# Kernel tuning notes

Hardware: AMD Instinct MI355X
Metric: run time of the kernel (lower is better)

## Reference

```python
import jax, jax.numpy as jnp
import numpy as np

B, D_IN, H, V_TOT, T = 131072, 128, 256, 6, 6  # total_vocab = vocab_size+1 = 6


def setup_inputs() -> dict:
    key = jax.random.key(0)
    ks = jax.random.split(key, 16)
    s = 0.02
    return {
        "x": jax.random.normal(ks[0], (B, D_IN), jnp.float32),
        "W_enc": jax.random.normal(ks[1], (D_IN, H), jnp.float32) * s,
        "b_enc": jnp.zeros((H,), jnp.float32),
        "W_embed": jax.random.normal(ks[2], (V_TOT, H), jnp.float32) * s,
        "b_embed": jnp.zeros((H,), jnp.float32),
        "W_z": jax.random.normal(ks[3], (2 * H, H), jnp.float32) * s,
        "b_z": jnp.zeros((H,), jnp.float32),
        "W_r": jax.random.normal(ks[4], (2 * H, H), jnp.float32) * s,
        "b_r": jnp.zeros((H,), jnp.float32),
        "W_h": jax.random.normal(ks[5], (2 * H, H), jnp.float32) * s,
        "b_h": jnp.zeros((H,), jnp.float32),
        "W_out": jax.random.normal(ks[6], (H, V_TOT), jnp.float32) * s,
        "b_out": jnp.zeros((V_TOT,), jnp.float32),
        "start_embed": jax.random.normal(ks[7], (H,), jnp.float32) * 0.01,
    }


def reference(x, W_enc, b_enc, W_embed, b_embed, W_z, b_z, W_r, b_r, W_h, b_h,
              W_out, b_out, start_embed):
    h0 = x @ W_enc + b_enc                      # encoder: (B, H)
    bsz = h0.shape[0]
    keys = jax.random.split(jax.random.key(42), T)

    def gru(xin, h):
        c = jnp.concatenate([xin, h], axis=-1)
        z = jax.nn.sigmoid(c @ W_z + b_z)
        r = jax.nn.sigmoid(c @ W_r + b_r)
        cr = jnp.concatenate([xin, r * h], axis=-1)
        h_t = jnp.tanh(cr @ W_h + b_h)
        return (1 - z) * h + z * h_t

    def step(carry, key_t):
        h, prev_embed, total_lp, stopped, lengths = carry
        h = gru(prev_embed, h)
        logits = h @ W_out + b_out              # (B, V_TOT)
        token = jax.random.categorical(key_t, logits)  # training=True sampling
        logp = jax.nn.log_softmax(logits)
        active = (~stopped).astype(logits.dtype)
        lp = jnp.take_along_axis(logp, token[:, None], axis=1)[:, 0] * active
        total_lp = total_lp + lp
        onehot = jax.nn.one_hot(token, V_TOT, dtype=logits.dtype) * active[:, None]
        is_stop = token == (V_TOT - 1)
        lengths = lengths + ((~stopped) & (~is_stop)).astype(jnp.int32)
        stopped = stopped | is_stop
        prev_embed = jax.lax.stop_gradient(onehot) @ W_embed + b_embed
        return (h, prev_embed, total_lp, stopped, lengths), onehot

    init = (h0,
            jnp.broadcast_to(start_embed, (bsz, H)),
            jnp.zeros((bsz,), h0.dtype),
            jnp.zeros((bsz,), bool),
            jnp.zeros((bsz,), jnp.int32))
    (h, _, total_log_prob, _, lengths), onehots = jax.lax.scan(step, init, keys)
    # onehots: (T, B, V_TOT) -> message (B, T*V_TOT)
    message = jnp.transpose(onehots, (1, 0, 2)).reshape(bsz, T * V_TOT)
    return message, total_log_prob, lengths
```

## Files before the change

### kernel.cpp

```cpp
#include <hip/hip_runtime.h>
#include <stdint.h>

#define NB   131072
#define DIN  128
#define HD   256
#define VT   6
#define TS   6
#define BM   32
#define NTH  256

typedef __attribute__((ext_vector_type(8))) short bfrag;
typedef __attribute__((ext_vector_type(4))) short bh4;
typedef __attribute__((ext_vector_type(4))) float f32x4;

struct Keys { uint32_t a[6]; uint32_t b[6]; };

#define HPS(p, kc, nt, lp, j) ((((p) * 8 + (kc)) * 1040) + (nt) * 512 + (lp) * 8 + (j))

__host__ __device__ inline void tf2x32(uint32_t k0, uint32_t k1,
                                       uint32_t c0, uint32_t c1,
                                       uint32_t& o0, uint32_t& o1) {
  uint32_t ks2 = k0 ^ k1 ^ 0x1BD11BDAu;
  uint32_t x0 = c0 + k0, x1 = c1 + k1;
#define TFR(d) { x0 += x1; x1 = (x1 << (d)) | (x1 >> (32 - (d))); x1 ^= x0; }
  TFR(13) TFR(15) TFR(26) TFR(6)
  x0 += k1;  x1 += ks2 + 1u;
  TFR(17) TFR(29) TFR(16) TFR(24)
  x0 += ks2; x1 += k0 + 2u;
  TFR(13) TFR(15) TFR(26) TFR(6)
  x0 += k0;  x1 += k1 + 3u;
  TFR(17) TFR(29) TFR(16) TFR(24)
  x0 += k1;  x1 += ks2 + 4u;
  TFR(13) TFR(15) TFR(26) TFR(6)
  x0 += ks2; x1 += k0 + 5u;
#undef TFR
  o0 = x0; o1 = x1;
}

__device__ __forceinline__ unsigned short f2bf(float x) {
  uint32_t b = __float_as_uint(x);
  uint32_t r = b + 0x7FFFu + ((b >> 16) & 1u);
  return (unsigned short)(r >> 16);
}
__device__ __forceinline__ float bf2f(unsigned short u) {
  return __uint_as_float(((uint32_t)u) << 16);
}
__device__ __forceinline__ float sigf(float v) { return 1.0f / (1.0f + expf(-v)); }

#define MFMA16(a, b, c) __builtin_amdgcn_mfma_f32_16x16x32_bf16((a), (b), (c), 0, 0, 0)

__device__ __forceinline__ f32x4 prod6(const bfrag A[3], bfrag B0, bfrag B1, bfrag B2,
                                       f32x4 c) {
  c = MFMA16(A[0], B0, c);
  c = MFMA16(A[0], B1, c);
  c = MFMA16(A[1], B0, c);
  c = MFMA16(A[1], B1, c);
  c = MFMA16(A[0], B2, c);
  c = MFMA16(A[2], B0, c);
  return c;
}

__global__ void pre_kernel(const float* __restrict__ W_enc,
                           const float* __restrict__ W_embed,
                           const float* __restrict__ b_embed,
                           const float* __restrict__ start_embed,
                           const float* __restrict__ W_z, const float* __restrict__ b_z,
                           const float* __restrict__ W_r, const float* __restrict__ b_r,
                           const float* __restrict__ W_h, const float* __restrict__ b_h,
                           const float* __restrict__ W_out,
                           float* __restrict__ pre,
                           unsigned short* __restrict__ encf,
                           unsigned short* __restrict__ zf,
                           unsigned short* __restrict__ rf,
                           unsigned short* __restrict__ hf,
                           unsigned short* __restrict__ woutf) {
  const int bid = blockIdx.x;
  if (bid < 24) {
    __shared__ float xin[HD];
    const int c = bid & 7, g = bid >> 3, j = threadIdx.x;
    float v;
    if (c < 6)       v = W_embed[c * HD + j] + b_embed[j];
    else if (c == 6) v = b_embed[j];
    else             v = start_embed[j];
    xin[j] = v;
    __syncthreads();
    const float* Wg = (g == 0) ? W_z : (g == 1) ? W_r : W_h;
    const float* bg = (g == 0) ? b_z : (g == 1) ? b_r : b_h;
    float acc = bg[j];
    for (int k = 0; k < HD; ++k) acc += xin[k] * Wg[k * HD + j];
    pre[(g * 8 + c) * HD + j] = acc;
    return;
  }
  if (bid >= 136) {
    int id2 = (bid - 136) * 256 + threadIdx.x;
    int kc = id2 >> 6, lane = id2 & 63;
    int m = lane & 15, k0 = kc * 32 + ((lane >> 4) & 3) * 8;
    __align__(16) unsigned short P[3][8];
#pragma unroll
    for (int j = 0; j < 8; ++j) {
      float w = (m < VT) ? W_out[(size_t)(k0 + j) * VT + m] : 0.f;
      unsigned short h1 = f2bf(w);  float r1 = w - bf2f(h1);
      unsigned short h2 = f2bf(r1); float r2 = r1 - bf2f(h2);
      P[0][j] = h1; P[1][j] = h2; P[2][j] = f2bf(r2);
    }
    for (int p = 0; p < 3; ++p) {
      unsigned short* d = woutf + ((size_t)(p * 8 + kc) * 512) + (size_t)lane * 8;
      *(uint4*)d = *(const uint4*)P[p];
    }
    return;
  }
  int id = (bid - 24) * 256 + threadIdx.x;
  const float* src; unsigned short* dst; int kc, mt, lane, KC, krow0;
  if (id < 4096) {
    lane = id & 63; mt = (id >> 6) & 15; kc = id >> 10;
    src = W_enc; dst = encf; KC = 4; krow0 = 0;
  } else {
    int rem = id - 4096; int g = rem >> 13; int rr = rem & 8191;
    lane = rr & 63; mt = (rr >> 6) & 15; kc = rr >> 10;
    src = (g == 0) ? W_z : (g == 1) ? W_r : W_h;
    dst = (g == 0) ? zf  : (g == 1) ? rf  : hf;
    KC = 8; krow0 = 256;
  }
  const int m  = mt * 16 + (lane & 15);
  const int k0 = kc * 32 + ((lane >> 4) & 3) * 8;
  __align__(16) unsigned short P[3][8];
#pragma unroll
  for (int j = 0; j < 8; ++j) {
    float w = src[(size_t)(krow0 + k0 + j) * HD + m];
    unsigned short h1 = f2bf(w);  float r1 = w - bf2f(h1);
    unsigned short h2 = f2bf(r1); float r2 = r1 - bf2f(h2);
    P[0][j] = h1; P[1][j] = h2; P[2][j] = f2bf(r2);
  }
  for (int p = 0; p < 3; ++p) {
    unsigned short* d = dst + ((size_t)(p * KC + kc) * 16 + mt) * 512 + (size_t)lane * 8;
    *(uint4*)d = *(const uint4*)P[p];
  }
}

template<int KC, int NG>
__device__ __forceinline__ void gemm_pass(const unsigned short* __restrict__ f0,
                                          const unsigned short* __restrict__ f1,
                                          const unsigned short* hp_s,
                                          int wave, int lane,
                                          f32x4 acc0[4][2], f32x4 acc1[4][2]) {
#pragma unroll 1
  for (int kc = 0; kc < KC; ++kc) {
    bfrag B[3][2];
#pragma unroll
    for (int p = 0; p < 3; ++p)
#pragma unroll
      for (int nt = 0; nt < 2; ++nt)
        B[p][nt] = *(const bfrag*)&hp_s[HPS(p, kc, nt, lane, 0)];
#pragma unroll
    for (int mtl = 0; mtl < 4; ++mtl) {
      const int fo = (kc * 16 + wave * 4 + mtl) * 512 + lane * 8;
      bfrag A0[3], A1[3];
#pragma unroll
      for (int p = 0; p < 3; ++p) A0[p] = *(const bfrag*)(f0 + fo + p * (KC * 8192));
      if (NG == 2) {
#pragma unroll
        for (int p = 0; p < 3; ++p) A1[p] = *(const bfrag*)(f1 + fo + p * (KC * 8192));
      }
#pragma unroll
      for (int nt = 0; nt < 2; ++nt) {
        acc0[mtl][nt] = prod6(A0, B[0][nt], B[1][nt], B[2][nt], acc0[mtl][nt]);
        if (NG == 2)
          acc1[mtl][nt] = prod6(A1, B[0][nt], B[1][nt], B[2][nt], acc1[mtl][nt]);
      }
    }
  }
}

__device__ __forceinline__ void gen_gumbel(float* __restrict__ gmb, int s, int b0,
                                           int tile, int lane,
                                           uint32_t ka, uint32_t kb) {
  uint32_t basej = (uint32_t)(b0 + tile * 16) * 6u;
#pragma unroll
  for (int rep = 0; rep < 2; ++rep) {
    int d = rep * 64 + lane;
    if (d < 96) {
      uint32_t o0, o1;
      tf2x32(ka, kb, 0u, basej + (uint32_t)d, o0, o1);
      uint32_t bits = o0 ^ o1;
      float f = __uint_as_float((bits >> 9) | 0x3f800000u) - 1.0f;
      float u = (f > 0.f) ? f : 1.175494350822288e-38f;
      float lg1 = (float)log((double)u);
      float lg2 = (float)log((double)(-lg1));
      gmb[((s & 1) * 32 + tile * 16 + d / 6) * 6 + (d % 6)] = -lg2;
    }
  }
}

__launch_bounds__(NTH, 2)
__global__ void main_kernel(const float* __restrict__ x,
                            const float* __restrict__ b_enc,
                            const float* __restrict__ b_out,
                            const float* __restrict__ pre,
                            const unsigned short* __restrict__ encf,
                            const unsigned short* __restrict__ zf,
                            const unsigned short* __restrict__ rf,
                            const unsigned short* __restrict__ hf,
                            const unsigned short* __restrict__ woutf,
                            float* __restrict__ out, Keys keys) {
  __shared__ __align__(16) unsigned short hp_s[3 * 8 * 1040];
  __shared__ float gmb_s[2 * 32 * 6];
  __shared__ float boutL[16];
  __shared__ unsigned state[BM];
  __shared__ float tlp[BM];

  const int tid = threadIdx.x;
  const int wave = tid >> 6, lane = tid & 63;
  const int ln = lane & 15, qk = lane >> 4;
  const int b0 = blockIdx.x * BM;

  if (tid < 16) boutL[tid] = (tid < VT) ? b_out[tid] : 0.f;
  if (tid < BM) { state[tid] = 7u; tlp[tid] = 0.f; }

  for (int i = tid; i < BM * DIN; i += NTH) {
    int row = i >> 7, k = i & 127;
    float v = x[(size_t)(b0 + row) * DIN + k];
    unsigned short h1 = f2bf(v);  float r1 = v - bf2f(h1);
    unsigned short h2 = f2bf(r1); float r2 = r1 - bf2f(h2);
    int kc = k >> 5, nt = row >> 4, lp = (row & 15) + 16 * ((k >> 3) & 3), j = k & 7;
    hp_s[HPS(0, kc, nt, lp, j)] = h1;
    hp_s[HPS(1, kc, nt, lp, j)] = h2;
    hp_s[HPS(2, kc, nt, lp, j)] = f2bf(r2);
  }
  if (wave >= 2) gen_gumbel(gmb_s, 0, b0, wave - 2, lane, keys.a[0], keys.b[0]);
  __syncthreads();

  f32x4 acc0[4][2], acc1[4][2], z_s[4][2], hold[4][2];

#pragma unroll
  for (int mtl = 0; mtl < 4; ++mtl) {
    int mb = (wave * 4 + mtl) * 16 + qk * 4;
    f32x4 be = *(const f32x4*)&b_enc[mb];
#pragma unroll
    for (int nt = 0; nt < 2; ++nt) acc0[mtl][nt] = be;
  }
  gemm_pass<4, 1>(encf, nullptr, hp_s, wave, lane, acc0, acc1);
  __syncthreads();
#pragma unroll
  for (int mtl = 0; mtl < 4; ++mtl) {
    int mb = (wave * 4 + mtl) * 16 + qk * 4;
    int kc = mb >> 5, hi2 = (mb >> 3) & 3, j0 = mb & 7, lp = ln + 16 * hi2;
#pragma unroll
    for (int nt = 0; nt < 2; ++nt) {
      f32x4 o = acc0[mtl][nt];
      hold[mtl][nt] = o;
      bh4 P0, P1, P2;
#pragma unroll
      for (int j = 0; j < 4; ++j) {
        float v = o[j];
        unsigned short h1 = f2bf(v);  float r1 = v - bf2f(h1);
        unsigned short h2 = f2bf(r1); float r2 = r1 - bf2f(h2);
        P0[j] = (short)h1; P1[j] = (short)h2; P2[j] = (short)f2bf(r2);
      }
      *(bh4*)&hp_s[HPS(0, kc, nt, lp, j0)] = P0;
      *(bh4*)&hp_s[HPS(1, kc, nt, lp, j0)] = P1;
      *(bh4*)&hp_s[HPS(2, kc, nt, lp, j0)] = P2;
    }
  }
  __syncthreads();

#pragma unroll 1
  for (int t = 0; t < TS; ++t) {
#pragma unroll
    for (int mtl = 0; mtl < 4; ++mtl) {
      int mb = (wave * 4 + mtl) * 16 + qk * 4;
#pragma unroll
      for (int nt = 0; nt < 2; ++nt) {
        int code = (int)(state[nt * 16 + ln] & 7u);
        acc0[mtl][nt] = *(const f32x4*)&pre[(0 * 8 + code) * 256 + mb];
        acc1[mtl][nt] = *(const f32x4*)&pre[(1 * 8 + code) * 256 + mb];
      }
    }
    gemm_pass<8, 2>(zf, rf, hp_s, wave, lane, acc0, acc1);
    __syncthreads();
#pragma unroll
    for (int mtl = 0; mtl < 4; ++mtl) {
      int mb = (wave * 4 + mtl) * 16 + qk * 4;
      int kc = mb >> 5, hi2 = (mb >> 3) & 3, j0 = mb & 7, lp = ln + 16 * hi2;
#pragma unroll
      for (int nt = 0; nt < 2; ++nt) {
        f32x4 ho = hold[mtl][nt];
        f32x4 zv;
        bh4 P0, P1, P2;
#pragma unroll
        for (int j = 0; j < 4; ++j) {
          zv[j] = sigf(acc0[mtl][nt][j]);
          float rhv = sigf(acc1[mtl][nt][j]) * ho[j];
          unsigned short h1 = f2bf(rhv); float r1 = rhv - bf2f(h1);
          unsigned short h2 = f2bf(r1);  float r2 = r1 - bf2f(h2);
          P0[j] = (short)h1; P1[j] = (short)h2; P2[j] = (short)f2bf(r2);
        }
        z_s[mtl][nt] = zv;
        *(bh4*)&hp_s[HPS(0, kc, nt, lp, j0)] = P0;
        *(bh4*)&hp_s[HPS(1, kc, nt, lp, j0)] = P1;
        *(bh4*)&hp_s[HPS(2, kc, nt, lp, j0)] = P2;
      }
    }
    __syncthreads();

#pragma unroll
    for (int mtl = 0; mtl < 4; ++mtl) {
      int mb = (wave * 4 + mtl) * 16 + qk * 4;
#pragma unroll
      for (int nt = 0; nt < 2; ++nt) {
        int code = (int)(state[nt * 16 + ln] & 7u);
        acc0[mtl][nt] = *(const f32x4*)&pre[(2 * 8 + code) * 256 + mb];
      }
    }
    gemm_pass<8, 1>(hf, nullptr, hp_s, wave, lane, acc0, acc1);
    __syncthreads();
#pragma unroll
    for (int mtl = 0; mtl < 4; ++mtl) {
      int mb = (wave * 4 + mtl) * 16 + qk * 4;
      int kc = mb >> 5, hi2 = (mb >> 3) & 3, j0 = mb & 7, lp = ln + 16 * hi2;
#pragma unroll
      for (int nt = 0; nt < 2; ++nt) {
        f32x4 z = z_s[mtl][nt], ho = hold[mtl][nt], hn;
        bh4 P0, P1, P2;
#pragma unroll
        for (int j = 0; j < 4; ++j) {
          float ht = tanhf(acc0[mtl][nt][j]);
          hn[j] = (1.0f - z[j]) * ho[j] + z[j] * ht;
          unsigned short h1 = f2bf(hn[j]); float r1 = hn[j] - bf2f(h1);
          unsigned short h2 = f2bf(r1);    float r2 = r1 - bf2f(h2);
          P0[j] = (short)h1; P1[j] = (short)h2; P2[j] = (short)f2bf(r2);
        }
        hold[mtl][nt] = hn;
        *(bh4*)&hp_s[HPS(0, kc, nt, lp, j0)] = P0;
        *(bh4*)&hp_s[HPS(1, kc, nt, lp, j0)] = P1;
        *(bh4*)&hp_s[HPS(2, kc, nt, lp, j0)] = P2;
      }
    }
    __syncthreads();

    if (wave < 2) {
      f32x4 lacc;
#pragma unroll
      for (int j = 0; j < 4; ++j) lacc[j] = boutL[qk * 4 + j];
#pragma unroll 1
      for (int kc = 0; kc < 8; ++kc) {
        bfrag B0 = *(const bfrag*)&hp_s[HPS(0, kc, wave, lane, 0)];
        bfrag B1 = *(const bfrag*)&hp_s[HPS(1, kc, wave, lane, 0)];
        bfrag B2 = *(const bfrag*)&hp_s[HPS(2, kc, wave, lane, 0)];
        bfrag A[3];
#pragma unroll
        for (int p = 0; p < 3; ++p)
          A[p] = *(const bfrag*)(woutf + (p * 8 + kc) * 512 + lane * 8);
        lacc = prod6(A, B0, B1, B2, lacc);
      }
      float l4 = __shfl(lacc[0], ln + 16, 64);
      float l5 = __shfl(lacc[1], ln + 16, 64);
      if (qk == 0) {
        const int m = wave * 16 + ln;
        const int row = b0 + m;
        unsigned st = state[m];
        if (!(st & 8u)) {
          float l[VT] = {lacc[0], lacc[1], lacc[2], lacc[3], l4, l5};
          float best = 0.f; int tok = 0;
#pragma unroll
          for (int v = 0; v < VT; ++v) {
            float val = l[v] + gmb_s[((t & 1) * 32 + m) * 6 + v];
            if (v == 0 || val > best) { best = val; tok = v; }
          }
          float lmax = l[0];
#pragma unroll
          for (int v = 1; v < VT; ++v) lmax = fmaxf(lmax, l[v]);
          float s = 0.f;
#pragma unroll
          for (int v = 0; v < VT; ++v) s += expf(l[v] - lmax);
          float lp = (l[tok] - lmax) - logf(s);
          tlp[m] += lp;
          const bool is_stop = (tok == VT - 1);
          unsigned len = ((st >> 4) & 7u) + (is_stop ? 0u : 1u);
#pragma unroll
          for (int v = 0; v < VT; ++v)
            out[(size_t)row * (TS * VT) + t * VT + v] = (v == tok) ? 1.0f : 0.0f;
          state[m] = (unsigned)tok | (is_stop ? 8u : 0u) | (len << 4);
        } else {
#pragma unroll
          for (int v = 0; v < VT; ++v)
            out[(size_t)row * (TS * VT) + t * VT + v] = 0.0f;
          state[m] = 6u | 8u | (st & 0x70u);
        }
      }
    } else if (t + 1 < TS) {
      gen_gumbel(gmb_s, t + 1, b0, wave - 2, lane, keys.a[t + 1], keys.b[t + 1]);
    }
    __syncthreads();
  }

  if (tid < BM) {
    const int row = b0 + tid;
    out[(size_t)NB * (TS * VT) + row]      = tlp[tid];
    out[(size_t)NB * (TS * VT) + NB + row] = (float)((state[tid] >> 4) & 7u);
  }
}

extern "C" void kernel_launch(void* const* d_in, const int* in_sizes, int n_in,
                              void* d_out, int out_size, void* d_ws, size_t ws_size,
                              hipStream_t stream) {
  (void)in_sizes; (void)n_in; (void)out_size; (void)ws_size;
  const float* x          = (const float*)d_in[0];
  const float* W_enc      = (const float*)d_in[1];
  const float* b_enc      = (const float*)d_in[2];
  const float* W_embed    = (const float*)d_in[3];
  const float* b_embed    = (const float*)d_in[4];
  const float* W_z        = (const float*)d_in[5];
  const float* b_z        = (const float*)d_in[6];
  const float* W_r        = (const float*)d_in[7];
  const float* b_r        = (const float*)d_in[8];
  const float* W_h        = (const float*)d_in[9];
  const float* b_h        = (const float*)d_in[10];
  const float* W_out      = (const float*)d_in[11];
  const float* b_out      = (const float*)d_in[12];
  const float* start_embed= (const float*)d_in[13];
  float* out = (float*)d_out;

  float* pre = (float*)d_ws;
  unsigned short* encf = (unsigned short*)((char*)d_ws + 24576);
  unsigned short* zfb  = (unsigned short*)((char*)d_ws + 221184);
  unsigned short* rfb  = (unsigned short*)((char*)d_ws + 614400);
  unsigned short* hfb  = (unsigned short*)((char*)d_ws + 1007616);
  unsigned short* wof  = (unsigned short*)((char*)d_ws + 1400832);

  pre_kernel<<<138, 256, 0, stream>>>(W_enc, W_embed, b_embed, start_embed,
                                      W_z, b_z, W_r, b_r, W_h, b_h, W_out,
                                      pre, encf, zfb, rfb, hfb, wof);

  Keys K;
  for (int t = 0; t < 6; ++t) {
    uint32_t o0, o1;
    tf2x32(0u, 42u, 0u, (uint32_t)t, o0, o1);
    K.a[t] = o0; K.b[t] = o1;
  }

  main_kernel<<<NB / BM, NTH, 0, stream>>>(x, b_enc, b_out,
                                           pre, encf, zfb, rfb, hfb, wof, out, K);
}
```

Baseline: 2.017 ms.

## Run two skewed 32-row groups per block to overlap GEMM and epilogue phases

Doubles the block to 512 threads and 64 rows, split into two independent 32-row groups with separate shared buffers. The kernel becomes a slot-driven phase machine in which group 1 runs one phase behind group 0. While one group is in a GEMM pass, the other is doing its elementwise or sampling phase, so the serial phases inside a block can overlap. In exchange, shared memory per block doubles, which may cut resident blocks per CU. Every slot still hits a block-wide barrier, and the branchy phase dispatch may add register pressure under launch_bounds(NTH,2).

```diff
diff --git a/kernel.cpp b/kernel.cpp
--- a/kernel.cpp
+++ b/kernel.cpp
@@ -6,8 +6,8 @@
 #define HD   256
 #define VT   6
 #define TS   6
-#define BM   32
-#define NTH  256
+#define BM   64
+#define NTH  512
 
 typedef __attribute__((ext_vector_type(8))) short bfrag;
 typedef __attribute__((ext_vector_type(4))) short bh4;
@@ -16,6 +16,7 @@
 struct Keys { uint32_t a[6]; uint32_t b[6]; };
 
 #define HPS(p, kc, nt, lp, j) ((((p) * 8 + (kc)) * 1040) + (nt) * 512 + (lp) * 8 + (j))
+#define HPHALF (3 * 8 * 1040)
 
 __host__ __device__ inline void tf2x32(uint32_t k0, uint32_t k1,
                                        uint32_t c0, uint32_t c1,
@@ -140,8 +141,8 @@
 template<int KC, int NG>
 __device__ __forceinline__ void gemm_pass(const unsigned short* __restrict__ f0,
                                           const unsigned short* __restrict__ f1,
-                                          const unsigned short* hp_s,
-                                          int wave, int lane,
+                                          const unsigned short* hp,
+                                          int w4, int lane,
                                           f32x4 acc0[4][2], f32x4 acc1[4][2]) {
 #pragma unroll 1
   for (int kc = 0; kc < KC; ++kc) {
@@ -150,10 +151,10 @@
     for (int p = 0; p < 3; ++p)
 #pragma unroll
       for (int nt = 0; nt < 2; ++nt)
-        B[p][nt] = *(const bfrag*)&hp_s[HPS(p, kc, nt, lane, 0)];
+        B[p][nt] = *(const bfrag*)&hp[HPS(p, kc, nt, lane, 0)];
 #pragma unroll
     for (int mtl = 0; mtl < 4; ++mtl) {
-      const int fo = (kc * 16 + wave * 4 + mtl) * 512 + lane * 8;
+      const int fo = (kc * 16 + w4 * 4 + mtl) * 512 + lane * 8;
       bfrag A0[3], A1[3];
 #pragma unroll
       for (int p = 0; p < 3; ++p) A0[p] = *(const bfrag*)(f0 + fo + p * (KC * 8192));
@@ -202,201 +203,212 @@
                             const unsigned short* __restrict__ hf,
                             const unsigned short* __restrict__ woutf,
                             float* __restrict__ out, Keys keys) {
-  __shared__ __align__(16) unsigned short hp_s[3 * 8 * 1040];
-  __shared__ float gmb_s[2 * 32 * 6];
+  __shared__ __align__(16) unsigned short hp_s[2 * HPHALF];
+  __shared__ float gmb_s[2 * 2 * 32 * 6];
   __shared__ float boutL[16];
-  __shared__ unsigned state[BM];
-  __shared__ float tlp[BM];
-
-  const int tid = threadIdx.x;
+  __shared__ unsigned state_s[2 * 32];
+  __shared__ float tlp_s[2 * 32];
+
+  const int tid  = threadIdx.x;
   const int wave = tid >> 6, lane = tid & 63;
-  const int ln = lane & 15, qk = lane >> 4;
-  const int b0 = blockIdx.x * BM;
-
-  if (tid < 16) boutL[tid] = (tid < VT) ? b_out[tid] : 0.f;
-  if (tid < BM) { state[tid] = 7u; tlp[tid] = 0.f; }
-
-  for (int i = tid; i < BM * DIN; i += NTH) {
-    int row = i >> 7, k = i & 127;
-    float v = x[(size_t)(b0 + row) * DIN + k];
-    unsigned short h1 = f2bf(v);  float r1 = v - bf2f(h1);
-    unsigned short h2 = f2bf(r1); float r2 = r1 - bf2f(h2);
-    int kc = k >> 5, nt = row >> 4, lp = (row & 15) + 16 * ((k >> 3) & 3), j = k & 7;
-    hp_s[HPS(0, kc, nt, lp, j)] = h1;
-    hp_s[HPS(1, kc, nt, lp, j)] = h2;
-    hp_s[HPS(2, kc, nt, lp, j)] = f2bf(r2);
-  }
-  if (wave >= 2) gen_gumbel(gmb_s, 0, b0, wave - 2, lane, keys.a[0], keys.b[0]);
-  __syncthreads();
+  const int grp  = wave >> 2;
+  const int w4   = wave & 3;
+  const int ln   = lane & 15, qk = lane >> 4;
+  const int tid4 = tid & 255;
+  const int b0   = blockIdx.x * BM + grp * 32;
+
+  unsigned short* hp   = hp_s    + grp * HPHALF;
+  float*          gmb  = gmb_s   + grp * (2 * 32 * 6);
+  unsigned*       stp  = state_s + grp * 32;
+  float*          tlpp = tlp_s   + grp * 32;
 
   f32x4 acc0[4][2], acc1[4][2], z_s[4][2], hold[4][2];
 
-#pragma unroll
-  for (int mtl = 0; mtl < 4; ++mtl) {
-    int mb = (wave * 4 + mtl) * 16 + qk * 4;
-    f32x4 be = *(const f32x4*)&b_enc[mb];
-#pragma unroll
-    for (int nt = 0; nt < 2; ++nt) acc0[mtl][nt] = be;
-  }
-  gemm_pass<4, 1>(encf, nullptr, hp_s, wave, lane, acc0, acc1);
-  __syncthreads();
-#pragma unroll
-  for (int mtl = 0; mtl < 4; ++mtl) {
-    int mb = (wave * 4 + mtl) * 16 + qk * 4;
-    int kc = mb >> 5, hi2 = (mb >> 3) & 3, j0 = mb & 7, lp = ln + 16 * hi2;
-#pragma unroll
-    for (int nt = 0; nt < 2; ++nt) {
-      f32x4 o = acc0[mtl][nt];
-      hold[mtl][nt] = o;
-      bh4 P0, P1, P2;
-#pragma unroll
-      for (int j = 0; j < 4; ++j) {
-        float v = o[j];
+#pragma unroll 1
+  for (int slot = 0; slot < 35; ++slot) {
+    const int ph = slot - grp;
+    if (ph == 0) {
+      if (tid4 < 16) boutL[tid4] = (tid4 < VT) ? b_out[tid4] : 0.f;
+      if (tid4 < 32) { stp[tid4] = 7u; tlpp[tid4] = 0.f; }
+      for (int i = tid4; i < 32 * DIN; i += 256) {
+        int row = i >> 7, k = i & 127;
+        float v = x[(size_t)(b0 + row) * DIN + k];
         unsigned short h1 = f2bf(v);  float r1 = v - bf2f(h1);
         unsigned short h2 = f2bf(r1); float r2 = r1 - bf2f(h2);
-        P0[j] = (short)h1; P1[j] = (short)h2; P2[j] = (short)f2bf(r2);
-      }
-      *(bh4*)&hp_s[HPS(0, kc, nt, lp, j0)] = P0;
-      *(bh4*)&hp_s[HPS(1, kc, nt, lp, j0)] = P1;
-      *(bh4*)&hp_s[HPS(2, kc, nt, lp, j0)] = P2;
-    }
-  }
-  __syncthreads();
-
+        int kc = k >> 5, nt = row >> 4, lp = (row & 15) + 16 * ((k >> 3) & 3), j = k & 7;
+        hp[HPS(0, kc, nt, lp, j)] = h1;
+        hp[HPS(1, kc, nt, lp, j)] = h2;
+        hp[HPS(2, kc, nt, lp, j)] = f2bf(r2);
+      }
+      if (w4 >= 2) gen_gumbel(gmb, 0, b0, w4 - 2, lane, keys.a[0], keys.b[0]);
+    } else if (ph == 1) {
+#pragma unroll
+      for (int mtl = 0; mtl < 4; ++mtl) {
+        int mb = (w4 * 4 + mtl) * 16 + qk * 4;
+        f32x4 be = *(const f32x4*)&b_enc[mb];
+#pragma unroll
+        for (int nt = 0; nt < 2; ++nt) acc0[mtl][nt] = be;
+      }
+      gemm_pass<4, 1>(encf, nullptr, hp, w4, lane, acc0, acc1);
+    } else if (ph == 2) {
+#pragma unroll
+      for (int mtl = 0; mtl < 4; ++mtl) {
+        int mb = (w4 * 4 + mtl) * 16 + qk * 4;
+        int kc = mb >> 5, hi2 = (mb >> 3) & 3, j0 = mb & 7, lp = ln + 16 * hi2;
+#pragma unroll
+        for (int nt = 0; nt < 2; ++nt) {
+          f32x4 o = acc0[mtl][nt];
+          hold[mtl][nt] = o;
+          bh4 P0, P1, P2;
+#pragma unroll
+          for (int j = 0; j < 4; ++j) {
+            float v = o[j];
+            unsigned short h1 = f2bf(v);  float r1 = v - bf2f(h1);
+            unsigned short h2 = f2bf(r1); float r2 = r1 - bf2f(h2);
+            P0[j] = (short)h1; P1[j] = (short)h2; P2[j] = (short)f2bf(r2);
+          }
+          *(bh4*)&hp[HPS(0, kc, nt, lp, j0)] = P0;
+          *(bh4*)&hp[HPS(1, kc, nt, lp, j0)] = P1;
+          *(bh4*)&hp[HPS(2, kc, nt, lp, j0)] = P2;
+        }
+      }
+    } else if (ph >= 3 && ph <= 32) {
+      const int q = ph - 3;
+      const int t = q / 5;
+      const int sub = q - t * 5;
+      if (sub == 0) {
+#pragma unroll
+        for (int mtl = 0; mtl < 4; ++mtl) {
+          int mb = (w4 * 4 + mtl) * 16 + qk * 4;
+#pragma unroll
+          for (int nt = 0; nt < 2; ++nt) {
+            int code = (int)(stp[nt * 16 + ln] & 7u);
+            acc0[mtl][nt] = *(const f32x4*)&pre[(0 * 8 + code) * 256 + mb];
+            acc1[mtl][nt] = *(const f32x4*)&pre[(1 * 8 + code) * 256 + mb];
+          }
+        }
+        gemm_pass<8, 2>(zf, rf, hp, w4, lane, acc0, acc1);
+      } else if (sub == 1) {
+#pragma unroll
+        for (int mtl = 0; mtl < 4; ++mtl) {
+          int mb = (w4 * 4 + mtl) * 16 + qk * 4;
+          int kc = mb >> 5, hi2 = (mb >> 3) & 3, j0 = mb & 7, lp = ln + 16 * hi2;
+#pragma unroll
+          for (int nt = 0; nt < 2; ++nt) {
+            f32x4 ho = hold[mtl][nt];
+            f32x4 zv;
+            bh4 P0, P1, P2;
+#pragma unroll
+            for (int j = 0; j < 4; ++j) {
+              zv[j] = sigf(acc0[mtl][nt][j]);
+              float rhv = sigf(acc1[mtl][nt][j]) * ho[j];
+              unsigned short h1 = f2bf(rhv); float r1 = rhv - bf2f(h1);
+              unsigned short h2 = f2bf(r1);  float r2 = r1 - bf2f(h2);
+              P0[j] = (short)h1; P1[j] = (short)h2; P2[j] = (short)f2bf(r2);
+            }
+            z_s[mtl][nt] = zv;
+            *(bh4*)&hp[HPS(0, kc, nt, lp, j0)] = P0;
+            *(bh4*)&hp[HPS(1, kc, nt, lp, j0)] = P1;
+            *(bh4*)&hp[HPS(2, kc, nt, lp, j0)] = P2;
+          }
+        }
+      } else if (sub == 2) {
+#pragma unroll
+        for (int mtl = 0; mtl < 4; ++mtl) {
+          int mb = (w4 * 4 + mtl) * 16 + qk * 4;
+#pragma unroll
+          for (int nt = 0; nt < 2; ++nt) {
+            int code = (int)(stp[nt * 16 + ln] & 7u);
+            acc0[mtl][nt] = *(const f32x4*)&pre[(2 * 8 + code) * 256 + mb];
+          }
+        }
+        gemm_pass<8, 1>(hf, nullptr, hp, w4, lane, acc0, acc1);
+      } else if (sub == 3) {
+#pragma unroll
+        for (int mtl = 0; mtl < 4; ++mtl) {
+          int mb = (w4 * 4 + mtl) * 16 + qk * 4;
+          int kc = mb >> 5, hi2 = (mb >> 3) & 3, j0 = mb & 7, lp = ln + 16 * hi2;
+#pragma unroll
+          for (int nt = 0; nt < 2; ++nt) {
+            f32x4 z = z_s[mtl][nt], ho = hold[mtl][nt], hn;
+            bh4 P0, P1, P2;
+#pragma unroll
+            for (int j = 0; j < 4; ++j) {
+              float ht = tanhf(acc0[mtl][nt][j]);
+              hn[j] = (1.0f - z[j]) * ho[j] + z[j] * ht;
+              unsigned short h1 = f2bf(hn[j]); float r1 = hn[j] - bf2f(h1);
+              unsigned short h2 = f2bf(r1);    float r2 = r1 - bf2f(h2);
+              P0[j] = (short)h1; P1[j] = (short)h2; P2[j] = (short)f2bf(r2);
+            }
+            hold[mtl][nt] = hn;
+            *(bh4*)&hp[HPS(0, kc, nt, lp, j0)] = P0;
+            *(bh4*)&hp[HPS(1, kc, nt, lp, j0)] = P1;
+            *(bh4*)&hp[HPS(2, kc, nt, lp, j0)] = P2;
+          }
+        }
+      } else {
+        if (w4 < 2) {
+          f32x4 lacc;
+#pragma unroll
+          for (int j = 0; j < 4; ++j) lacc[j] = boutL[qk * 4 + j];
 #pragma unroll 1
-  for (int t = 0; t < TS; ++t) {
-#pragma unroll
-    for (int mtl = 0; mtl < 4; ++mtl) {
-      int mb = (wave * 4 + mtl) * 16 + qk * 4;
-#pragma unroll
-      for (int nt = 0; nt < 2; ++nt) {
-        int code = (int)(state[nt * 16 + ln] & 7u);
-        acc0[mtl][nt] = *(const f32x4*)&pre[(0 * 8 + code) * 256 + mb];
-        acc1[mtl][nt] = *(const f32x4*)&pre[(1 * 8 + code) * 256 + mb];
-      }
-    }
-    gemm_pass<8, 2>(zf, rf, hp_s, wave, lane, acc0, acc1);
-    __syncthreads();
-#pragma unroll
-    for (int mtl = 0; mtl < 4; ++mtl) {
-      int mb = (wave * 4 + mtl) * 16 + qk * 4;
-      int kc = mb >> 5, hi2 = (mb >> 3) & 3, j0 = mb & 7, lp = ln + 16 * hi2;
-#pragma unroll
-      for (int nt = 0; nt < 2; ++nt) {
-        f32x4 ho = hold[mtl][nt];
-        f32x4 zv;
-        bh4 P0, P1, P2;
-#pragma unroll
-        for (int j = 0; j < 4; ++j) {
-          zv[j] = sigf(acc0[mtl][nt][j]);
-          float rhv = sigf(acc1[mtl][nt][j]) * ho[j];
-          unsigned short h1 = f2bf(rhv); float r1 = rhv - bf2f(h1);
-          unsigned short h2 = f2bf(r1);  float r2 = r1 - bf2f(h2);
-          P0[j] = (short)h1; P1[j] = (short)h2; P2[j] = (short)f2bf(r2);
-        }
-        z_s[mtl][nt] = zv;
-        *(bh4*)&hp_s[HPS(0, kc, nt, lp, j0)] = P0;
-        *(bh4*)&hp_s[HPS(1, kc, nt, lp, j0)] = P1;
-        *(bh4*)&hp_s[HPS(2, kc, nt, lp, j0)] = P2;
+          for (int kc = 0; kc < 8; ++kc) {
+            bfrag B0 = *(const bfrag*)&hp[HPS(0, kc, w4, lane, 0)];
+            bfrag B1 = *(const bfrag*)&hp[HPS(1, kc, w4, lane, 0)];
+            bfrag B2 = *(const bfrag*)&hp[HPS(2, kc, w4, lane, 0)];
+            bfrag A[3];
+#pragma unroll
+            for (int p = 0; p < 3; ++p)
+              A[p] = *(const bfrag*)(woutf + (p * 8 + kc) * 512 + lane * 8);
+            lacc = prod6(A, B0, B1, B2, lacc);
+          }
+          float l4 = __shfl(lacc[0], ln + 16, 64);
+          float l5 = __shfl(lacc[1], ln + 16, 64);
+          if (qk == 0) {
+            const int m = w4 * 16 + ln;
+            const int row = b0 + m;
+            unsigned st = stp[m];
+            if (!(st & 8u)) {
+              float l[VT] = {lacc[0], lacc[1], lacc[2], lacc[3], l4, l5};
+              float best = 0.f; int tok = 0;
+#pragma unroll
+              for (int v = 0; v < VT; ++v) {
+                float val = l[v] + gmb[((t & 1) * 32 + m) * 6 + v];
+                if (v == 0 || val > best) { best = val; tok = v; }
+              }
+              float lmax = l[0];
+#pragma unroll
+              for (int v = 1; v < VT; ++v) lmax = fmaxf(lmax, l[v]);
+              float s = 0.f;
+#pragma unroll
+              for (int v = 0; v < VT; ++v) s += expf(l[v] - lmax);
+              float lp = (l[tok] - lmax) - logf(s);
+              tlpp[m] += lp;
+              const bool is_stop = (tok == VT - 1);
+              unsigned len = ((st >> 4) & 7u) + (is_stop ? 0u : 1u);
+#pragma unroll
+              for (int v = 0; v < VT; ++v)
+                out[(size_t)row * (TS * VT) + t * VT + v] = (v == tok) ? 1.0f : 0.0f;
+              stp[m] = (unsigned)tok | (is_stop ? 8u : 0u) | (len << 4);
+            } else {
+#pragma unroll
+              for (int v = 0; v < VT; ++v)
+                out[(size_t)row * (TS * VT) + t * VT + v] = 0.0f;
+              stp[m] = 6u | 8u | (st & 0x70u);
+            }
+          }
+        } else if (t + 1 < TS) {
+          gen_gumbel(gmb, t + 1, b0, w4 - 2, lane, keys.a[t + 1], keys.b[t + 1]);
+        }
+      }
+    } else if (ph == 33) {
+      if (tid4 < 32) {
+        const int row = b0 + tid4;
+        out[(size_t)NB * (TS * VT) + row]      = tlpp[tid4];
+        out[(size_t)NB * (TS * VT) + NB + row] = (float)((stp[tid4] >> 4) & 7u);
       }
     }
     __syncthreads();
-
-#pragma unroll
-    for (int mtl = 0; mtl < 4; ++mtl) {
-      int mb = (wave * 4 + mtl) * 16 + qk * 4;
-#pragma unroll
-      for (int nt = 0; nt < 2; ++nt) {
-        int code = (int)(state[nt * 16 + ln] & 7u);
-        acc0[mtl][nt] = *(const f32x4*)&pre[(2 * 8 + code) * 256 + mb];
-      }
-    }
-    gemm_pass<8, 1>(hf, nullptr, hp_s, wave, lane, acc0, acc1);
-    __syncthreads();
-#pragma unroll
-    for (int mtl = 0; mtl < 4; ++mtl) {
-      int mb = (wave * 4 + mtl) * 16 + qk * 4;
-      int kc = mb >> 5, hi2 = (mb >> 3) & 3, j0 = mb & 7, lp = ln + 16 * hi2;
-#pragma unroll
-      for (int nt = 0; nt < 2; ++nt) {
-        f32x4 z = z_s[mtl][nt], ho = hold[mtl][nt], hn;
-        bh4 P0, P1, P2;
-#pragma unroll
-        for (int j = 0; j < 4; ++j) {
-          float ht = tanhf(acc0[mtl][nt][j]);
-          hn[j] = (1.0f - z[j]) * ho[j] + z[j] * ht;
-          unsigned short h1 = f2bf(hn[j]); float r1 = hn[j] - bf2f(h1);
-          unsigned short h2 = f2bf(r1);    float r2 = r1 - bf2f(h2);
-          P0[j] = (short)h1; P1[j] = (short)h2; P2[j] = (short)f2bf(r2);
-        }
-        hold[mtl][nt] = hn;
-        *(bh4*)&hp_s[HPS(0, kc, nt, lp, j0)] = P0;
-        *(bh4*)&hp_s[HPS(1, kc, nt, lp, j0)] = P1;
-        *(bh4*)&hp_s[HPS(2, kc, nt, lp, j0)] = P2;
-      }
-    }
-    __syncthreads();
-
-    if (wave < 2) {
-      f32x4 lacc;
-#pragma unroll
-      for (int j = 0; j < 4; ++j) lacc[j] = boutL[qk * 4 + j];
-#pragma unroll 1
-      for (int kc = 0; kc < 8; ++kc) {
-        bfrag B0 = *(const bfrag*)&hp_s[HPS(0, kc, wave, lane, 0)];
-        bfrag B1 = *(const bfrag*)&hp_s[HPS(1, kc, wave, lane, 0)];
-        bfrag B2 = *(const bfrag*)&hp_s[HPS(2, kc, wave, lane, 0)];
-        bfrag A[3];
-#pragma unroll
-        for (int p = 0; p < 3; ++p)
-          A[p] = *(const bfrag*)(woutf + (p * 8 + kc) * 512 + lane * 8);
-        lacc = prod6(A, B0, B1, B2, lacc);
-      }
-      float l4 = __shfl(lacc[0], ln + 16, 64);
-      float l5 = __shfl(lacc[1], ln + 16, 64);
-      if (qk == 0) {
-        const int m = wave * 16 + ln;
-        const int row = b0 + m;
-        unsigned st = state[m];
-        if (!(st & 8u)) {
-          float l[VT] = {lacc[0], lacc[1], lacc[2], lacc[3], l4, l5};
-          float best = 0.f; int tok = 0;
-#pragma unroll
-          for (int v = 0; v < VT; ++v) {
-            float val = l[v] + gmb_s[((t & 1) * 32 + m) * 6 + v];
-            if (v == 0 || val > best) { best = val; tok = v; }
-          }
-          float lmax = l[0];
-#pragma unroll
-          for (int v = 1; v < VT; ++v) lmax = fmaxf(lmax, l[v]);
-          float s = 0.f;
-#pragma unroll
-          for (int v = 0; v < VT; ++v) s += expf(l[v] - lmax);
-          float lp = (l[tok] - lmax) - logf(s);
-          tlp[m] += lp;
-          const bool is_stop = (tok == VT - 1);
-          unsigned len = ((st >> 4) & 7u) + (is_stop ? 0u : 1u);
-#pragma unroll
-          for (int v = 0; v < VT; ++v)
-            out[(size_t)row * (TS * VT) + t * VT + v] = (v == tok) ? 1.0f : 0.0f;
-          state[m] = (unsigned)tok | (is_stop ? 8u : 0u) | (len << 4);
-        } else {
-#pragma unroll
-          for (int v = 0; v < VT; ++v)
-            out[(size_t)row * (TS * VT) + t * VT + v] = 0.0f;
-          state[m] = 6u | 8u | (st & 0x70u);
-        }
-      }
-    } else if (t + 1 < TS) {
-      gen_gumbel(gmb_s, t + 1, b0, wave - 2, lane, keys.a[t + 1], keys.b[t + 1]);
-    }
-    __syncthreads();
-  }
-
-  if (tid < BM) {
-    const int row = b0 + tid;
-    out[(size_t)NB * (TS * VT) + row]      = tlp[tid];
-    out[(size_t)NB * (TS * VT) + NB + row] = (float)((state[tid] >> 4) & 7u);
   }
 }
 
```

Result: slower. 6.832 ms (+238.7%).
